# Performance work log

Hardware: AMD Instinct MI355X
Metric: run time of the kernel (lower is better)

Reference implementation:

```python
import jax, jax.numpy as jnp
import numpy as np
import math

DIM = 1024
H = 16
DK = DIM // H
SEG = 512
NN = 2      # num_neighbors
DIL = 4     # dilation
B, L = 2, 8192


def setup_inputs() -> dict:
    key = jax.random.key(0)
    ks = jax.random.split(key, 9)
    scale = 1.0 / math.sqrt(DIM)
    def lin(k):
        return jax.random.normal(k, (DIM, DIM), jnp.float32) * scale
    return {
        "x": jax.random.normal(ks[0], (B, L, DIM), jnp.float32),
        "Wq": lin(ks[1]), "bq": jnp.zeros((DIM,), jnp.float32),
        "Wk": lin(ks[2]), "bk": jnp.zeros((DIM,), jnp.float32),
        "Wv": lin(ks[3]), "bv": jnp.zeros((DIM,), jnp.float32),
        "Wo": lin(ks[4]), "bo": jnp.zeros((DIM,), jnp.float32),
    }


def _attn(q, k, v):
    # q: [B,S,H,Q,dk], k/v: [B,S,H,K,dk]
    scores = jnp.einsum('bshqd,bshkd->bshqk', q, k) / math.sqrt(q.shape[-1])
    a = jax.nn.softmax(scores, axis=-1)
    return jnp.einsum('bshqk,bshkd->bshqd', a, v)


def reference(x, Wq, bq, Wk, bk, Wv, bv, Wo, bo):
    Bx, Lx, C = x.shape
    pad = (-Lx) % SEG

    def proj_chunk(W, b):
        t = x @ W + b                                  # [B,L,C]
        t = jnp.pad(t, ((0, 0), (0, pad), (0, 0)))
        S = t.shape[1] // SEG
        t = t.reshape(Bx, S, SEG, H, DK)
        return t.transpose(0, 1, 3, 2, 4)              # [B,S,H,seg,dk]

    q = proj_chunk(Wq, bq)
    k = proj_chunk(Wk, bk)
    v = proj_chunk(Wv, bv)
    S = q.shape[1]

    # segment-local dense attention (vectorized over all segments)
    out = _attn(q, k, v)

    # dilated sampling of neighbor segments' keys/values
    dil_idx = jnp.arange(0, SEG, DIL)
    kd = k[:, :, :, dil_idx, :]                        # [B,S,H,seg/DIL,dk]
    vd = v[:, :, :, dil_idx, :]

    seg_ids = jnp.arange(S)
    w = 1.0 / (2 * NN)
    for off in range(1, NN + 1):
        for sign in (-1, 1):
            n = seg_ids + sign * off
            valid = (n >= 0) & (n < S)                 # [S]
            nc = jnp.clip(n, 0, S - 1)
            cross = _attn(q, kd[:, nc], vd[:, nc])     # [B,S,H,seg,dk]
            out = out + jnp.where(valid[None, :, None, None, None], cross * w, 0.0)

    out = out.transpose(0, 1, 3, 2, 4).reshape(Bx, S * SEG, C)
    out = out[:, :Lx, :]
    return out @ Wo + bo
```

## Files before the change

### kernel.cpp

```cpp
#include <hip/hip_runtime.h>
#include <stdint.h>

typedef __attribute__((ext_vector_type(8))) short short8;
typedef __attribute__((ext_vector_type(4))) float f32x4;

#define MFMA16(A_, B_, C_) __builtin_amdgcn_mfma_f32_16x16x32_bf16((A_), (B_), (C_), 0, 0, 0)

#if __has_builtin(__builtin_amdgcn_exp2f)
#define EXP2(x) __builtin_amdgcn_exp2f(x)
#else
#define EXP2(x) exp2f(x)
#endif

#define GLDS16(g_, l_)                                                        \
  __builtin_amdgcn_global_load_lds(                                           \
      (const __attribute__((address_space(1))) void*)(g_),                    \
      (__attribute__((address_space(3))) void*)(l_), 16, 0, 0)

__device__ __forceinline__ unsigned short f2bf(float f) {
  unsigned int u = __float_as_uint(f);
  u += 0x7fffu + ((u >> 16) & 1u);
  return (unsigned short)(u >> 16);
}

__device__ __forceinline__ unsigned pk2(float a, float b) {
  return (__float_as_uint(a) >> 16) | (__float_as_uint(b) & 0xffff0000u);
}


__global__ void cast_x_kernel(const float* __restrict__ x,
                              unsigned short* __restrict__ xb, int n4) {
  int i = blockIdx.x * blockDim.x + threadIdx.x;
  if (i >= n4) return;
  float4 v = reinterpret_cast<const float4*>(x)[i];
  uint2 pk;
  pk.x = (unsigned)f2bf(v.x) | ((unsigned)f2bf(v.y) << 16);
  pk.y = (unsigned)f2bf(v.z) | ((unsigned)f2bf(v.w) << 16);
  reinterpret_cast<uint2*>(xb)[i] = pk;
}

__global__ void transpose_cast_kernel(const float* __restrict__ W,
                                      unsigned short* __restrict__ Wt) {
  __shared__ float tile[32][33];
  int k0 = blockIdx.x * 32, n0 = blockIdx.y * 32;
  int tx = threadIdx.x, ty = threadIdx.y;
  for (int i = ty; i < 32; i += 8)
    tile[i][tx] = W[(size_t)(k0 + i) * 1024 + n0 + tx];
  __syncthreads();
  for (int i = ty; i < 32; i += 8)
    Wt[(size_t)(n0 + i) * 1024 + k0 + tx] = f2bf(tile[tx][i]);
}

template<int MODE>
__global__ __launch_bounds__(512, 2) void gemm_kernel(
    const unsigned short* __restrict__ A,
    const unsigned short* __restrict__ W,
    const float* __restrict__ bias,
    unsigned short* __restrict__ out_bf,
    unsigned short* __restrict__ out_vtd,
    float* __restrict__ out_f) {
  __shared__ unsigned short Asm[2][256 * 64];
  __shared__ unsigned short Bsm[2][256 * 64];
  const int t = threadIdx.x;
  const int wg = (blockIdx.x & 7) * 32 + (blockIdx.x >> 3);
  const int m0 = (wg >> 2) * 256;
  const int n0 = (wg & 3) * 256;
  const int w = t >> 6, lane = t & 63, lr = lane & 15, lg = lane >> 4;
  const int wm = w >> 2, wn = w & 3;

  f32x4 acc[8][4];
#pragma unroll
  for (int i = 0; i < 8; ++i)
#pragma unroll
    for (int j = 0; j < 4; ++j) acc[i][j] = f32x4{0.f, 0.f, 0.f, 0.f};

  const int srow = lane >> 3;
  const int sswz = ((lane & 7) ^ srow) * 8;
  const unsigned short* gA = A + (size_t)(m0 + w * 32 + srow) * 1024 + sswz;
  const unsigned short* gB = W + (size_t)(n0 + w * 32 + srow) * 1024 + sswz;

  auto stage = [&](int buf, int kt) {
    const unsigned short* ga = gA + kt * 64;
    const unsigned short* gb = gB + kt * 64;
    unsigned short* la = &Asm[buf][(w * 32) * 64];
    unsigned short* lb = &Bsm[buf][(w * 32) * 64];
#pragma unroll
    for (int p = 0; p < 4; ++p) {
      GLDS16(ga + (size_t)(p * 8) * 1024, la + p * 8 * 64);
      GLDS16(gb + (size_t)(p * 8) * 1024, lb + p * 8 * 64);
    }
  };

  const int rswz = (lr & 7);
  auto compute = [&](int buf) {
    const unsigned short* bA = &Asm[buf][0];
    const unsigned short* bB = &Bsm[buf][0];
    short8 bfv[2][4];
#pragma unroll
    for (int ks = 0; ks < 2; ++ks)
#pragma unroll
      for (int j = 0; j < 4; ++j) {
        const int row = wn * 64 + j * 16 + lr;
        bfv[ks][j] = *reinterpret_cast<const short8*>(
            &bB[row * 64 + (((ks * 4 + lg) ^ rswz) * 8)]);
      }
#pragma unroll
    for (int i = 0; i < 8; ++i) {
      const int row = wm * 128 + i * 16 + lr;
      short8 af[2];
#pragma unroll
      for (int ks = 0; ks < 2; ++ks)
        af[ks] = *reinterpret_cast<const short8*>(
            &bA[row * 64 + (((ks * 4 + lg) ^ rswz) * 8)]);
#pragma unroll
      for (int ks = 0; ks < 2; ++ks)
#pragma unroll
        for (int j = 0; j < 4; ++j)
          acc[i][j] = MFMA16(af[ks], bfv[ks][j], acc[i][j]);
    }
  };

  stage(0, 0);
#pragma unroll 1
  for (int kt = 0; kt < 15; ++kt) {
    stage((kt + 1) & 1, kt + 1);
    asm volatile("s_waitcnt vmcnt(8)\n\ts_barrier" ::: "memory");
    compute(kt & 1);
    asm volatile("s_waitcnt lgkmcnt(0)\n\ts_barrier" ::: "memory");
  }
  asm volatile("s_waitcnt vmcnt(0)\n\ts_barrier" ::: "memory");
  compute(1);

#pragma unroll
  for (int i = 0; i < 8; ++i)
#pragma unroll
    for (int j = 0; j < 4; ++j) {
      const int n = n0 + wn * 64 + j * 16 + lr;
      const float bv = bias[n];
#pragma unroll
      for (int r = 0; r < 4; ++r) {
        const int m = m0 + wm * 128 + i * 16 + lg * 4 + r;
        float val = acc[i][j][r] + bv;
        if (MODE == 3) {
          out_f[(size_t)m * 1024 + n] = val;
        } else {
          const int b = m >> 13, ll = m & 8191;
          const int ss = ll >> 9, rr = ll & 511;
          const int hh = n >> 6, d = n & 63;
          const size_t head = (size_t)((b * 16 + ss) * 16 + hh);
          if (MODE == 0) {
            out_bf[head * 32768 + rr * 64 + d] = f2bf(val * 0.18033688011112042f);
          } else if (MODE == 1) {
            out_bf[head * 32768 + rr * 64 + d] = f2bf(val);
          } else {
            const int p32 = (((rr >> 2) & 3) << 3) | (((rr >> 4) & 1) << 2) | (rr & 3);
            out_bf[head * 32768 + (size_t)d * 512 + ((rr & ~31) | p32)] = f2bf(val);
            if ((rr & 3) == 0) {
              const int cd = rr >> 2;
              const int pd = (((cd >> 2) & 3) << 3) | (((cd >> 4) & 1) << 2) | (cd & 3);
              out_vtd[head * 8192 + (size_t)d * 128 + ((cd & ~31) | pd)] = f2bf(val);
            }
          }
        }
      }
    }
}

__device__ __forceinline__ void attn_group(
    const unsigned short* __restrict__ Kp, int kstride,
    const unsigned short* __restrict__ Vp, int vstride,
    int nchunks, float wgt,
    const short8 (&qf)[2][2],
    unsigned short* __restrict__ Kl, unsigned short* __restrict__ Vl,
    f32x4 (&total)[2][4],
    int lr, int lg, int w, int lane) {
  const int srow = lane >> 3;
  const int fcw = (lane & 7) ^ srow;
  const unsigned short* gK = Kp + (size_t)(w * 16 + srow) * kstride + fcw * 8;
  const unsigned short* gV = Vp + (size_t)(w * 16 + srow) * vstride + fcw * 8;
  const int sxk = (lr & 7) * 8;

  float l[2][2] = {{0.f, 0.f}, {0.f, 0.f}};
  f32x4 acc[2][4];
#pragma unroll
  for (int rt = 0; rt < 2; ++rt)
#pragma unroll
    for (int dt = 0; dt < 4; ++dt) acc[rt][dt] = f32x4{0.f, 0.f, 0.f, 0.f};

  {
    unsigned short* dk = Kl + w * 1024;
    unsigned short* dv = Vl + w * 1024;
    GLDS16(gK, dk); GLDS16(gK + 8 * kstride, dk + 512);
    GLDS16(gV, dv); GLDS16(gV + 8 * vstride, dv + 512);
  }
  __syncthreads();

  int cur = 0;
  for (int c = 0; c < nchunks; ++c) {
    if (c + 1 < nchunks) {
      const unsigned short* gk = gK + (size_t)((c + 1) * 64) * kstride;
      const unsigned short* gv = gV + (c + 1) * 64;
      unsigned short* dk = Kl + (cur ^ 1) * 4096 + w * 1024;
      unsigned short* dv = Vl + (cur ^ 1) * 4096 + w * 1024;
      GLDS16(gk, dk); GLDS16(gk + 8 * kstride, dk + 512);
      GLDS16(gv, dv); GLDS16(gv + 8 * vstride, dv + 512);
    }
    const unsigned short* bK = Kl + cur * 4096;
    const unsigned short* bV = Vl + cur * 4096;

    short8 pf[2][2];
#pragma unroll
    for (int kp = 0; kp < 2; ++kp) {
      f32x4 s0[2], s1[2];
#pragma unroll
      for (int rt = 0; rt < 2; ++rt) {
        s0[rt] = f32x4{0.f, 0.f, 0.f, 0.f};
        s1[rt] = f32x4{0.f, 0.f, 0.f, 0.f};
      }
      __builtin_amdgcn_s_setprio(1);
#pragma unroll
      for (int ks = 0; ks < 2; ++ks) {
        const int rc = ((ks * 4 + lg) * 8) ^ sxk;
        short8 kf0 = *reinterpret_cast<const short8*>(&bK[(kp * 32 + lr) * 64 + rc]);
        short8 kf1 = *reinterpret_cast<const short8*>(&bK[(kp * 32 + 16 + lr) * 64 + rc]);
#pragma unroll
        for (int rt = 0; rt < 2; ++rt) {
          s0[rt] = MFMA16(kf0, qf[rt][ks], s0[rt]);
          s1[rt] = MFMA16(kf1, qf[rt][ks], s1[rt]);
        }
      }
      __builtin_amdgcn_s_setprio(0);
#pragma unroll
      for (int rt = 0; rt < 2; ++rt) {
        float e0 = EXP2(s0[rt][0]), e1 = EXP2(s0[rt][1]);
        float e2 = EXP2(s0[rt][2]), e3 = EXP2(s0[rt][3]);
        float e4 = EXP2(s1[rt][0]), e5 = EXP2(s1[rt][1]);
        float e6 = EXP2(s1[rt][2]), e7 = EXP2(s1[rt][3]);
        l[rt][kp] += ((e0 + e1) + (e2 + e3)) + ((e4 + e5) + (e6 + e7));
        uint4 wv;
        wv.x = pk2(e0, e1); wv.y = pk2(e2, e3);
        wv.z = pk2(e4, e5); wv.w = pk2(e6, e7);
        pf[rt][kp] = *reinterpret_cast<short8*>(&wv);
      }
    }
    __builtin_amdgcn_s_setprio(1);
#pragma unroll
    for (int ks = 0; ks < 2; ++ks) {
      const int rcv = ((ks * 4 + lg) * 8) ^ sxk;
#pragma unroll
      for (int dt = 0; dt < 4; ++dt) {
        short8 vf = *reinterpret_cast<const short8*>(&bV[(dt * 16 + lr) * 64 + rcv]);
#pragma unroll
        for (int rt = 0; rt < 2; ++rt)
          acc[rt][dt] = MFMA16(pf[rt][ks], vf, acc[rt][dt]);
      }
    }
    __builtin_amdgcn_s_setprio(0);
    __syncthreads();
    cur ^= 1;
  }
#pragma unroll
  for (int rt = 0; rt < 2; ++rt) {
    float s = l[rt][0] + l[rt][1];
    s += __shfl_xor(s, 16);
    s += __shfl_xor(s, 32);
    float rl[4];
#pragma unroll
    for (int r = 0; r < 4; ++r) rl[r] = wgt / __shfl(s, lg * 4 + r);
#pragma unroll
    for (int dt = 0; dt < 4; ++dt)
#pragma unroll
      for (int r = 0; r < 4; ++r) total[rt][dt][r] += acc[rt][dt][r] * rl[r];
  }
}

__global__ __launch_bounds__(256) void attn_kernel(
    const unsigned short* __restrict__ Q,
    const unsigned short* __restrict__ K,
    const unsigned short* __restrict__ Vt,
    const unsigned short* __restrict__ Vtd,
    unsigned short* __restrict__ AO) {
  __shared__ unsigned short Kl[2 * 4096];
  __shared__ unsigned short Vl[2 * 4096];
  const int wg = blockIdx.x;
  const int qb = wg & 3;
  const int bsh = wg >> 2;
  const int h = bsh & 15, s = (bsh >> 4) & 15, b = bsh >> 8;
  const int t = threadIdx.x, w = t >> 6, lane = t & 63, lr = lane & 15, lg = lane >> 4;
  const int q0 = qb * 128 + w * 32;

  const size_t headbase = (size_t)((b * 16 + s) * 16 + h);
  const unsigned short* Qp = Q + headbase * 32768 + (size_t)q0 * 64;
  short8 qf[2][2];
#pragma unroll
  for (int rt = 0; rt < 2; ++rt)
#pragma unroll
    for (int ks = 0; ks < 2; ++ks)
      qf[rt][ks] = *reinterpret_cast<const short8*>(&Qp[(rt * 16 + lr) * 64 + ks * 32 + lg * 8]);

  f32x4 total[2][4];
#pragma unroll
  for (int rt = 0; rt < 2; ++rt)
#pragma unroll
    for (int dt = 0; dt < 4; ++dt) total[rt][dt] = f32x4{0.f, 0.f, 0.f, 0.f};

  attn_group(K + headbase * 32768, 64, Vt + headbase * 32768, 512, 8, 1.0f,
             qf, Kl, Vl, total, lr, lg, w, lane);
#pragma unroll
  for (int gi = 0; gi < 4; ++gi) {
    const int off = (gi == 0) ? -2 : (gi == 1) ? -1 : (gi == 2) ? 1 : 2;
    const int ns = s + off;
    if (ns < 0 || ns > 15) continue;
    const size_t hb = (size_t)((b * 16 + ns) * 16 + h);
    attn_group(K + hb * 32768, 256, Vtd + hb * 8192, 128, 2, 0.25f,
               qf, Kl, Vl, total, lr, lg, w, lane);
  }
  const size_t obase = ((size_t)b * 8192 + (size_t)s * 512 + q0) * 1024 + h * 64;
#pragma unroll
  for (int rt = 0; rt < 2; ++rt)
#pragma unroll
    for (int dt = 0; dt < 4; ++dt)
#pragma unroll
      for (int r = 0; r < 4; ++r) {
        const int q = rt * 16 + lg * 4 + r;
        const int d = dt * 16 + lr;
        AO[obase + (size_t)q * 1024 + d] = f2bf(total[rt][dt][r]);
      }
}

extern "C" void kernel_launch(void* const* d_in, const int* in_sizes, int n_in,
                              void* d_out, int out_size, void* d_ws, size_t ws_size,
                              hipStream_t stream) {
  const float* x  = (const float*)d_in[0];
  const float* Wq = (const float*)d_in[1];
  const float* bq = (const float*)d_in[2];
  const float* Wk = (const float*)d_in[3];
  const float* bk = (const float*)d_in[4];
  const float* Wv = (const float*)d_in[5];
  const float* bv = (const float*)d_in[6];
  const float* Wo = (const float*)d_in[7];
  const float* bo = (const float*)d_in[8];
  float* out = (float*)d_out;

  char* ws = (char*)d_ws;
  unsigned short* Xb   = (unsigned short*)(ws);
  unsigned short* Wqt  = (unsigned short*)(ws + 33554432);
  unsigned short* Wkt  = (unsigned short*)(ws + 35651584);
  unsigned short* Wvt  = (unsigned short*)(ws + 37748736);
  unsigned short* Wot  = (unsigned short*)(ws + 39845888);
  unsigned short* Qb   = (unsigned short*)(ws + 41943040);
  unsigned short* Kb   = (unsigned short*)(ws + 75497472);
  unsigned short* Vtb  = (unsigned short*)(ws + 109051904);
  unsigned short* Vtdb = (unsigned short*)(ws + 142606336);
  unsigned short* AOb  = (unsigned short*)(ws + 150994944);

  cast_x_kernel<<<16384, 256, 0, stream>>>(x, Xb, 4194304);
  dim3 tb(32, 8), tg(32, 32);
  transpose_cast_kernel<<<tg, tb, 0, stream>>>(Wq, Wqt);
  transpose_cast_kernel<<<tg, tb, 0, stream>>>(Wk, Wkt);
  transpose_cast_kernel<<<tg, tb, 0, stream>>>(Wv, Wvt);
  transpose_cast_kernel<<<tg, tb, 0, stream>>>(Wo, Wot);

  gemm_kernel<0><<<256, 512, 0, stream>>>(Xb, Wqt, bq, Qb, nullptr, nullptr);
  gemm_kernel<1><<<256, 512, 0, stream>>>(Xb, Wkt, bk, Kb, nullptr, nullptr);
  gemm_kernel<2><<<256, 512, 0, stream>>>(Xb, Wvt, bv, Vtb, Vtdb, nullptr);

  attn_kernel<<<2048, 256, 0, stream>>>(Qb, Kb, Vtb, Vtdb, AOb);

  gemm_kernel<3><<<256, 512, 0, stream>>>(AOb, Wot, bo, nullptr, nullptr, out);
}
```

Baseline: 300.8 us.

## Interleave GEMM staging with MFMA phases and double attention block size

The GEMM main loop is restructured so each K-tile is split into four phases. Each phase reads two A row-tiles from LDS and issues their MFMAs at raised priority, and the next tile's global-to-LDS loads are split in two halves spread across the phases. This aims to overlap memory traffic with compute and drop the trailing epilogue compute. Separately, the attention kernel moves to 512-thread blocks covering 256 queries with half as many blocks, so each K/V chunk in LDS is shared by twice as many waves, at the cost of more barriers and fewer resident workgroups.

Result: slower. 324.9 us (+8.0%).

```diff
diff --git a/kernel.cpp b/kernel.cpp
--- a/kernel.cpp
+++ b/kernel.cpp
@@ -79,23 +79,58 @@
   const unsigned short* gA = A + (size_t)(m0 + w * 32 + srow) * 1024 + sswz;
   const unsigned short* gB = W + (size_t)(n0 + w * 32 + srow) * 1024 + sswz;
 
-  auto stage = [&](int buf, int kt) {
+  auto stageHalf = [&](int buf, int kt, int half) {
     const unsigned short* ga = gA + kt * 64;
     const unsigned short* gb = gB + kt * 64;
     unsigned short* la = &Asm[buf][(w * 32) * 64];
     unsigned short* lb = &Bsm[buf][(w * 32) * 64];
 #pragma unroll
-    for (int p = 0; p < 4; ++p) {
+    for (int p = half * 2; p < half * 2 + 2; ++p) {
       GLDS16(ga + (size_t)(p * 8) * 1024, la + p * 8 * 64);
       GLDS16(gb + (size_t)(p * 8) * 1024, lb + p * 8 * 64);
     }
   };
 
   const int rswz = (lr & 7);
-  auto compute = [&](int buf) {
+
+  stageHalf(0, 0, 0);
+  stageHalf(0, 0, 1);
+
+#pragma unroll 1
+  for (int kt = 0; kt < 16; ++kt) {
+    const int buf = kt & 1;
     const unsigned short* bA = &Asm[buf][0];
     const unsigned short* bB = &Bsm[buf][0];
-    short8 bfv[2][4];
+    short8 bfv[2][4], af[2][2];
+
+    auto readA2 = [&](int i0) {
+#pragma unroll
+      for (int ii = 0; ii < 2; ++ii)
+#pragma unroll
+        for (int ks = 0; ks < 2; ++ks) {
+          const int row = wm * 128 + (i0 + ii) * 16 + lr;
+          af[ii][ks] = *reinterpret_cast<const short8*>(
+              &bA[row * 64 + (((ks * 4 + lg) ^ rswz) * 8)]);
+        }
+    };
+    auto mfma16x = [&](int i0) {
+      __builtin_amdgcn_s_setprio(1);
+#pragma unroll
+      for (int ii = 0; ii < 2; ++ii)
+#pragma unroll
+        for (int ks = 0; ks < 2; ++ks)
+#pragma unroll
+          for (int j = 0; j < 4; ++j)
+            acc[i0 + ii][j] = MFMA16(af[ii][ks], bfv[ks][j], acc[i0 + ii][j]);
+      __builtin_amdgcn_s_setprio(0);
+    };
+
+    if (kt < 15) {
+      stageHalf(buf ^ 1, kt + 1, 0);
+      asm volatile("s_waitcnt vmcnt(4)\n\ts_barrier" ::: "memory");
+    } else {
+      asm volatile("s_waitcnt vmcnt(0)\n\ts_barrier" ::: "memory");
+    }
 #pragma unroll
     for (int ks = 0; ks < 2; ++ks)
 #pragma unroll
@@ -104,32 +139,30 @@
         bfv[ks][j] = *reinterpret_cast<const short8*>(
             &bB[row * 64 + (((ks * 4 + lg) ^ rswz) * 8)]);
       }
-#pragma unroll
-    for (int i = 0; i < 8; ++i) {
-      const int row = wm * 128 + i * 16 + lr;
-      short8 af[2];
-#pragma unroll
-      for (int ks = 0; ks < 2; ++ks)
-        af[ks] = *reinterpret_cast<const short8*>(
-            &bA[row * 64 + (((ks * 4 + lg) ^ rswz) * 8)]);
-#pragma unroll
-      for (int ks = 0; ks < 2; ++ks)
-#pragma unroll
-        for (int j = 0; j < 4; ++j)
-          acc[i][j] = MFMA16(af[ks], bfv[ks][j], acc[i][j]);
-    }
-  };
-
-  stage(0, 0);
-#pragma unroll 1
-  for (int kt = 0; kt < 15; ++kt) {
-    stage((kt + 1) & 1, kt + 1);
-    asm volatile("s_waitcnt vmcnt(8)\n\ts_barrier" ::: "memory");
-    compute(kt & 1);
-    asm volatile("s_waitcnt lgkmcnt(0)\n\ts_barrier" ::: "memory");
+    readA2(0);
+    asm volatile("s_waitcnt lgkmcnt(0)" ::: "memory");
+    mfma16x(0);
+    __builtin_amdgcn_s_barrier();
+
+    readA2(2);
+    if (kt < 15) stageHalf(buf ^ 1, kt + 1, 1);
+    __builtin_amdgcn_s_barrier();
+    asm volatile("s_waitcnt lgkmcnt(0)" ::: "memory");
+    mfma16x(2);
+    __builtin_amdgcn_s_barrier();
+
+    readA2(4);
+    __builtin_amdgcn_s_barrier();
+    asm volatile("s_waitcnt lgkmcnt(0)" ::: "memory");
+    mfma16x(4);
+    __builtin_amdgcn_s_barrier();
+
+    readA2(6);
+    __builtin_amdgcn_s_barrier();
+    asm volatile("s_waitcnt lgkmcnt(0)" ::: "memory");
+    mfma16x(6);
+    __builtin_amdgcn_s_barrier();
   }
-  asm volatile("s_waitcnt vmcnt(0)\n\ts_barrier" ::: "memory");
-  compute(1);
 
 #pragma unroll
   for (int i = 0; i < 8; ++i)
@@ -176,8 +209,8 @@
     int lr, int lg, int w, int lane) {
   const int srow = lane >> 3;
   const int fcw = (lane & 7) ^ srow;
-  const unsigned short* gK = Kp + (size_t)(w * 16 + srow) * kstride + fcw * 8;
-  const unsigned short* gV = Vp + (size_t)(w * 16 + srow) * vstride + fcw * 8;
+  const unsigned short* gK = Kp + (size_t)(w * 8 + srow) * kstride + fcw * 8;
+  const unsigned short* gV = Vp + (size_t)(w * 8 + srow) * vstride + fcw * 8;
   const int sxk = (lr & 7) * 8;
 
   float l[2][2] = {{0.f, 0.f}, {0.f, 0.f}};
@@ -187,23 +220,15 @@
 #pragma unroll
     for (int dt = 0; dt < 4; ++dt) acc[rt][dt] = f32x4{0.f, 0.f, 0.f, 0.f};
 
-  {
-    unsigned short* dk = Kl + w * 1024;
-    unsigned short* dv = Vl + w * 1024;
-    GLDS16(gK, dk); GLDS16(gK + 8 * kstride, dk + 512);
-    GLDS16(gV, dv); GLDS16(gV + 8 * vstride, dv + 512);
-  }
+  GLDS16(gK, Kl + w * 512);
+  GLDS16(gV, Vl + w * 512);
   __syncthreads();
 
   int cur = 0;
   for (int c = 0; c < nchunks; ++c) {
     if (c + 1 < nchunks) {
-      const unsigned short* gk = gK + (size_t)((c + 1) * 64) * kstride;
-      const unsigned short* gv = gV + (c + 1) * 64;
-      unsigned short* dk = Kl + (cur ^ 1) * 4096 + w * 1024;
-      unsigned short* dv = Vl + (cur ^ 1) * 4096 + w * 1024;
-      GLDS16(gk, dk); GLDS16(gk + 8 * kstride, dk + 512);
-      GLDS16(gv, dv); GLDS16(gv + 8 * vstride, dv + 512);
+      GLDS16(gK + (size_t)((c + 1) * 64) * kstride, Kl + (cur ^ 1) * 4096 + w * 512);
+      GLDS16(gV + (c + 1) * 64, Vl + (cur ^ 1) * 4096 + w * 512);
     }
     const unsigned short* bK = Kl + cur * 4096;
     const unsigned short* bV = Vl + cur * 4096;
@@ -274,7 +299,7 @@
   }
 }
 
-__global__ __launch_bounds__(256) void attn_kernel(
+__global__ __launch_bounds__(512) void attn_kernel(
     const unsigned short* __restrict__ Q,
     const unsigned short* __restrict__ K,
     const unsigned short* __restrict__ Vt,
@@ -283,11 +308,11 @@
   __shared__ unsigned short Kl[2 * 4096];
   __shared__ unsigned short Vl[2 * 4096];
   const int wg = blockIdx.x;
-  const int qb = wg & 3;
-  const int bsh = wg >> 2;
+  const int qh = wg & 1;
+  const int bsh = wg >> 1;
   const int h = bsh & 15, s = (bsh >> 4) & 15, b = bsh >> 8;
   const int t = threadIdx.x, w = t >> 6, lane = t & 63, lr = lane & 15, lg = lane >> 4;
-  const int q0 = qb * 128 + w * 32;
+  const int q0 = qh * 256 + w * 32;
 
   const size_t headbase = (size_t)((b * 16 + s) * 16 + h);
   const unsigned short* Qp = Q + headbase * 32768 + (size_t)q0 * 64;
@@ -365,7 +390,7 @@
   gemm_kernel<1><<<256, 512, 0, stream>>>(Xb, Wkt, bk, Kb, nullptr, nullptr);
   gemm_kernel<2><<<256, 512, 0, stream>>>(Xb, Wvt, bv, Vtb, Vtdb, nullptr);
 
-  attn_kernel<<<2048, 256, 0, stream>>>(Qb, Kb, Vtb, Vtdb, AOb);
+  attn_kernel<<<1024, 512, 0, stream>>>(Qb, Kb, Vtb, Vtdb, AOb);
 
   gemm_kernel<3><<<256, 512, 0, stream>>>(AOb, Wot, bo, nullptr, nullptr, out);
 }
```

## Process a whole segment per block with 8 waves and 64 query rows each

Applied to the files above, without the earlier changes.

The attention kernel now launches one 512-thread block per (batch, segment, head) instead of four 256-thread blocks. Each wave handles 64 query rows, so every K/V tile staged into shared memory is reused by the whole segment's queries rather than being reloaded by four separate blocks. The QK, softmax and PV steps are interleaved per row tile, and V fragments are loaded once per key half. The change also simplifies the LDS swizzle. The cost is more accumulator registers per lane and fewer, larger blocks (512 in total), which may reduce occupancy and latency hiding.

Result: slower. 321.0 us (+6.7%).

```diff
diff --git a/kernel.cpp b/kernel.cpp
--- a/kernel.cpp
+++ b/kernel.cpp
@@ -170,98 +170,80 @@
     const unsigned short* __restrict__ Kp, int kstride,
     const unsigned short* __restrict__ Vp, int vstride,
     int nchunks, float wgt,
-    const short8 (&qf)[2][2],
+    const short8 (&qf)[4][2],
     unsigned short* __restrict__ Kl, unsigned short* __restrict__ Vl,
-    f32x4 (&total)[2][4],
+    f32x4 (&total)[4][4],
     int lr, int lg, int w, int lane) {
   const int srow = lane >> 3;
   const int fcw = (lane & 7) ^ srow;
-  const unsigned short* gK = Kp + (size_t)(w * 16 + srow) * kstride + fcw * 8;
-  const unsigned short* gV = Vp + (size_t)(w * 16 + srow) * vstride + fcw * 8;
-  const int sxk = (lr & 7) * 8;
-
-  float l[2][2] = {{0.f, 0.f}, {0.f, 0.f}};
-  f32x4 acc[2][4];
-#pragma unroll
-  for (int rt = 0; rt < 2; ++rt)
+  const unsigned short* gK = Kp + (size_t)(w * 8 + srow) * kstride + fcw * 8;
+  const unsigned short* gV = Vp + (size_t)(w * 8 + srow) * vstride + fcw * 8;
+  const int sx = lr & 7;
+
+  float l[4] = {0.f, 0.f, 0.f, 0.f};
+  f32x4 acc[4][4];
+#pragma unroll
+  for (int rt = 0; rt < 4; ++rt)
 #pragma unroll
     for (int dt = 0; dt < 4; ++dt) acc[rt][dt] = f32x4{0.f, 0.f, 0.f, 0.f};
 
-  {
-    unsigned short* dk = Kl + w * 1024;
-    unsigned short* dv = Vl + w * 1024;
-    GLDS16(gK, dk); GLDS16(gK + 8 * kstride, dk + 512);
-    GLDS16(gV, dv); GLDS16(gV + 8 * vstride, dv + 512);
-  }
+  GLDS16(gK, Kl + w * 512);
+  GLDS16(gV, Vl + w * 512);
   __syncthreads();
 
   int cur = 0;
   for (int c = 0; c < nchunks; ++c) {
     if (c + 1 < nchunks) {
-      const unsigned short* gk = gK + (size_t)((c + 1) * 64) * kstride;
-      const unsigned short* gv = gV + (c + 1) * 64;
-      unsigned short* dk = Kl + (cur ^ 1) * 4096 + w * 1024;
-      unsigned short* dv = Vl + (cur ^ 1) * 4096 + w * 1024;
-      GLDS16(gk, dk); GLDS16(gk + 8 * kstride, dk + 512);
-      GLDS16(gv, dv); GLDS16(gv + 8 * vstride, dv + 512);
+      GLDS16(gK + (size_t)((c + 1) * 64) * kstride, Kl + (cur ^ 1) * 4096 + w * 512);
+      GLDS16(gV + (c + 1) * 64, Vl + (cur ^ 1) * 4096 + w * 512);
     }
     const unsigned short* bK = Kl + cur * 4096;
     const unsigned short* bV = Vl + cur * 4096;
 
-    short8 pf[2][2];
 #pragma unroll
     for (int kp = 0; kp < 2; ++kp) {
-      f32x4 s0[2], s1[2];
-#pragma unroll
-      for (int rt = 0; rt < 2; ++rt) {
-        s0[rt] = f32x4{0.f, 0.f, 0.f, 0.f};
-        s1[rt] = f32x4{0.f, 0.f, 0.f, 0.f};
-      }
-      __builtin_amdgcn_s_setprio(1);
+      short8 kf0[2], kf1[2], vf[4];
 #pragma unroll
       for (int ks = 0; ks < 2; ++ks) {
-        const int rc = ((ks * 4 + lg) * 8) ^ sxk;
-        short8 kf0 = *reinterpret_cast<const short8*>(&bK[(kp * 32 + lr) * 64 + rc]);
-        short8 kf1 = *reinterpret_cast<const short8*>(&bK[(kp * 32 + 16 + lr) * 64 + rc]);
-#pragma unroll
-        for (int rt = 0; rt < 2; ++rt) {
-          s0[rt] = MFMA16(kf0, qf[rt][ks], s0[rt]);
-          s1[rt] = MFMA16(kf1, qf[rt][ks], s1[rt]);
+        const int rc = (((ks * 4 + lg) ^ sx) * 8);
+        kf0[ks] = *reinterpret_cast<const short8*>(&bK[(kp * 32 + lr) * 64 + rc]);
+        kf1[ks] = *reinterpret_cast<const short8*>(&bK[(kp * 32 + 16 + lr) * 64 + rc]);
+      }
+      const int rcv = (((kp * 4 + lg) ^ sx) * 8);
+#pragma unroll
+      for (int dt = 0; dt < 4; ++dt)
+        vf[dt] = *reinterpret_cast<const short8*>(&bV[(dt * 16 + lr) * 64 + rcv]);
+#pragma unroll
+      for (int rt = 0; rt < 4; ++rt) {
+        f32x4 s0 = f32x4{0.f, 0.f, 0.f, 0.f};
+        f32x4 s1 = f32x4{0.f, 0.f, 0.f, 0.f};
+        __builtin_amdgcn_s_setprio(1);
+#pragma unroll
+        for (int ks = 0; ks < 2; ++ks) {
+          s0 = MFMA16(kf0[ks], qf[rt][ks], s0);
+          s1 = MFMA16(kf1[ks], qf[rt][ks], s1);
         }
-      }
-      __builtin_amdgcn_s_setprio(0);
-#pragma unroll
-      for (int rt = 0; rt < 2; ++rt) {
-        float e0 = EXP2(s0[rt][0]), e1 = EXP2(s0[rt][1]);
-        float e2 = EXP2(s0[rt][2]), e3 = EXP2(s0[rt][3]);
-        float e4 = EXP2(s1[rt][0]), e5 = EXP2(s1[rt][1]);
-        float e6 = EXP2(s1[rt][2]), e7 = EXP2(s1[rt][3]);
-        l[rt][kp] += ((e0 + e1) + (e2 + e3)) + ((e4 + e5) + (e6 + e7));
+        __builtin_amdgcn_s_setprio(0);
+        float e0 = EXP2(s0[0]), e1 = EXP2(s0[1]), e2 = EXP2(s0[2]), e3 = EXP2(s0[3]);
+        float e4 = EXP2(s1[0]), e5 = EXP2(s1[1]), e6 = EXP2(s1[2]), e7 = EXP2(s1[3]);
+        l[rt] += ((e0 + e1) + (e2 + e3)) + ((e4 + e5) + (e6 + e7));
         uint4 wv;
         wv.x = pk2(e0, e1); wv.y = pk2(e2, e3);
         wv.z = pk2(e4, e5); wv.w = pk2(e6, e7);
-        pf[rt][kp] = *reinterpret_cast<short8*>(&wv);
-      }
-    }
-    __builtin_amdgcn_s_setprio(1);
-#pragma unroll
-    for (int ks = 0; ks < 2; ++ks) {
-      const int rcv = ((ks * 4 + lg) * 8) ^ sxk;
-#pragma unroll
-      for (int dt = 0; dt < 4; ++dt) {
-        short8 vf = *reinterpret_cast<const short8*>(&bV[(dt * 16 + lr) * 64 + rcv]);
-#pragma unroll
-        for (int rt = 0; rt < 2; ++rt)
-          acc[rt][dt] = MFMA16(pf[rt][ks], vf, acc[rt][dt]);
-      }
-    }
-    __builtin_amdgcn_s_setprio(0);
+        short8 pf = *reinterpret_cast<short8*>(&wv);
+        __builtin_amdgcn_s_setprio(1);
+#pragma unroll
+        for (int dt = 0; dt < 4; ++dt)
+          acc[rt][dt] = MFMA16(pf, vf[dt], acc[rt][dt]);
+        __builtin_amdgcn_s_setprio(0);
+      }
+    }
     __syncthreads();
     cur ^= 1;
   }
 #pragma unroll
-  for (int rt = 0; rt < 2; ++rt) {
-    float s = l[rt][0] + l[rt][1];
+  for (int rt = 0; rt < 4; ++rt) {
+    float s = l[rt];
     s += __shfl_xor(s, 16);
     s += __shfl_xor(s, 32);
     float rl[4];
@@ -274,7 +256,7 @@
   }
 }
 
-__global__ __launch_bounds__(256) void attn_kernel(
+__global__ __launch_bounds__(512, 2) void attn_kernel(
     const unsigned short* __restrict__ Q,
     const unsigned short* __restrict__ K,
     const unsigned short* __restrict__ Vt,
@@ -282,25 +264,23 @@
     unsigned short* __restrict__ AO) {
   __shared__ unsigned short Kl[2 * 4096];
   __shared__ unsigned short Vl[2 * 4096];
-  const int wg = blockIdx.x;
-  const int qb = wg & 3;
-  const int bsh = wg >> 2;
+  const int bsh = blockIdx.x;
   const int h = bsh & 15, s = (bsh >> 4) & 15, b = bsh >> 8;
   const int t = threadIdx.x, w = t >> 6, lane = t & 63, lr = lane & 15, lg = lane >> 4;
-  const int q0 = qb * 128 + w * 32;
+  const int q0 = w * 64;
 
   const size_t headbase = (size_t)((b * 16 + s) * 16 + h);
   const unsigned short* Qp = Q + headbase * 32768 + (size_t)q0 * 64;
-  short8 qf[2][2];
-#pragma unroll
-  for (int rt = 0; rt < 2; ++rt)
+  short8 qf[4][2];
+#pragma unroll
+  for (int rt = 0; rt < 4; ++rt)
 #pragma unroll
     for (int ks = 0; ks < 2; ++ks)
       qf[rt][ks] = *reinterpret_cast<const short8*>(&Qp[(rt * 16 + lr) * 64 + ks * 32 + lg * 8]);
 
-  f32x4 total[2][4];
-#pragma unroll
-  for (int rt = 0; rt < 2; ++rt)
+  f32x4 total[4][4];
+#pragma unroll
+  for (int rt = 0; rt < 4; ++rt)
 #pragma unroll
     for (int dt = 0; dt < 4; ++dt) total[rt][dt] = f32x4{0.f, 0.f, 0.f, 0.f};
 
@@ -317,7 +297,7 @@
   }
   const size_t obase = ((size_t)b * 8192 + (size_t)s * 512 + q0) * 1024 + h * 64;
 #pragma unroll
-  for (int rt = 0; rt < 2; ++rt)
+  for (int rt = 0; rt < 4; ++rt)
 #pragma unroll
     for (int dt = 0; dt < 4; ++dt)
 #pragma unroll
@@ -365,7 +345,7 @@
   gemm_kernel<1><<<256, 512, 0, stream>>>(Xb, Wkt, bk, Kb, nullptr, nullptr);
   gemm_kernel<2><<<256, 512, 0, stream>>>(Xb, Wvt, bv, Vtb, Vtdb, nullptr);
 
-  attn_kernel<<<2048, 256, 0, stream>>>(Qb, Kb, Vtb, Vtdb, AOb);
+  attn_kernel<<<512, 512, 0, stream>>>(Qb, Kb, Vtb, Vtdb, AOb);
 
   gemm_kernel<3><<<256, 512, 0, stream>>>(AOb, Wot, bo, nullptr, nullptr, out);
 }
```
